# Performance work log

Hardware: AMD Instinct MI355X
Metric: run time of the kernel (lower is better)

## Reference

```python
import jax, jax.numpy as jnp
import numpy as np

B, P, D = 8, 1024, 1024
H, N = 16, 64  # num_heads, head_dim


def setup_inputs() -> dict:
    key = jax.random.key(0)
    k1, k2, k3 = jax.random.split(key, 3)
    inputs = jax.random.normal(k1, (B, P, D), dtype=jnp.float32)
    # Keras 'random_normal' initializer: stddev 0.05
    w_qkv = jax.random.normal(k2, (H, 3, D, N), dtype=jnp.float32) * 0.05
    w_o = jax.random.normal(k3, (N * H, D), dtype=jnp.float32) * 0.05
    return {"inputs": inputs, "w_qkv": w_qkv, "w_o": w_o}


def reference(inputs, w_qkv, w_o):
    # Per-head QKV projection: [b,p,d] x [h,3,d,n] -> [b,h,3,p,n]
    proj = jnp.einsum('bpv,havn->bhapn', inputs, w_qkv)
    q = proj[:, :, 0]  # [b,h,p,n]
    k = proj[:, :, 1]
    v = proj[:, :, 2]
    head_dim = q.shape[-1]
    scale = 1.0 / jnp.sqrt(jnp.asarray(head_dim, dtype=jnp.float32))
    scores = jnp.einsum('bhqn,bhkn->bhqk', q, k) * scale  # [b,h,p,p]
    attn = jax.nn.softmax(scores, axis=-1)
    out = jnp.einsum('bhqk,bhkn->bhqn', attn, v)  # [b,h,p,n]
    # concat heads along feature dim: [b,p,h*n]
    b, h, p, n = out.shape
    concat = out.transpose(0, 2, 1, 3).reshape(b, p, h * n)
    return jnp.einsum('bpi,ij->bpj', concat, w_o)  # [b,p,d_model]
```

## Files before the change

### kernel.cpp

```cpp
#include <hip/hip_runtime.h>
#include <stdint.h>

typedef _Float16 f16;
typedef __attribute__((ext_vector_type(2))) _Float16 f16x2;
typedef __attribute__((ext_vector_type(4))) _Float16 f16x4;
typedef __attribute__((ext_vector_type(8))) _Float16 f16x8;
typedef __attribute__((ext_vector_type(4))) float f32x4;
typedef __attribute__((ext_vector_type(4))) uint32_t u32x4;

__device__ __forceinline__ void gload_lds16(const void* g, void* l) {
  __builtin_amdgcn_global_load_lds(
      (__attribute__((address_space(1))) void*)const_cast<void*>(g),
      (__attribute__((address_space(3))) void*)l, 16, 0, 0);
}


__global__ void convert_x(const float* __restrict__ in, f16* __restrict__ out) {
  int i = blockIdx.x * 256 + threadIdx.x;
  float4 v = ((const float4*)in)[i];
  f16x4 hv;
  hv[0] = (f16)v.x; hv[1] = (f16)v.y; hv[2] = (f16)v.z; hv[3] = (f16)v.w;
  ((f16x4*)out)[i] = hv;
}

__global__ void transpose_wqkv(const float* __restrict__ in, f16* __restrict__ out) {
  __shared__ float tile[64][65];
  int s = blockIdx.x >> 4;
  int vt = blockIdx.x & 15;
  int hh = s / 3, a = s - hh * 3;
  int tx = threadIdx.x & 63, ty = threadIdx.x >> 6;
#pragma unroll
  for (int i = 0; i < 16; i++) {
    int r = i * 4 + ty;
    tile[r][tx] = in[((size_t)(s * 1024 + vt * 64 + r)) * 64 + tx];
  }
  __syncthreads();
#pragma unroll
  for (int i = 0; i < 16; i++) {
    int n = i * 4 + ty;
    out[((size_t)(a * 1024 + hh * 64 + n)) * 1024 + vt * 64 + tx] = (f16)tile[tx][n];
  }
}

__global__ void transpose_wo(const float* __restrict__ in, f16* __restrict__ out) {
  __shared__ float tile[64][65];
  int rt = blockIdx.x >> 4, ct = blockIdx.x & 15;
  int tx = threadIdx.x & 63, ty = threadIdx.x >> 6;
#pragma unroll
  for (int i = 0; i < 16; i++) {
    int r = i * 4 + ty;
    tile[r][tx] = in[((size_t)(rt * 64 + r)) * 1024 + ct * 64 + tx];
  }
  __syncthreads();
#pragma unroll
  for (int i = 0; i < 16; i++) {
    int j = i * 4 + ty;
    out[((size_t)(ct * 64 + j)) * 1024 + rt * 64 + tx] = (f16)tile[tx][j];
  }
}

__global__ __launch_bounds__(512, 2) void gemm_qkv_kernel(
    const f16* __restrict__ A, const f16* __restrict__ BT, f16* __restrict__ out,
    f16* __restrict__ VT) {
  constexpr int K = 1024;
  __shared__ __align__(16) f16 smem[73728];
  const int t = threadIdx.x;
  const int lane = t & 63, wave = t >> 6;
  const int lr = lane & 15, lg = lane >> 4;
  const int wm = wave >> 1, wn = wave & 1;
  const int bid = blockIdx.x;
  const int wg = (bid & 7) * 96 + (bid >> 3);
  const int bm = wg / 24, bn = wg % 24;
  const f16* Ab = A + (size_t)bm * 256 * K;
  const f16* Bb = BT + (size_t)bn * 128 * K;

  auto STAGE = [&](int kt, int buf) {
    const f16* srcA = Ab + kt * 64;
    char* dstA = (char*)(smem + buf * 16384);
#pragma unroll
    for (int i = 0; i < 4; i++) {
      int g = i * 512 + t;
      int r = g >> 3, p = g & 7;
      gload_lds16(srcA + (size_t)r * K + ((p ^ (r & 7)) << 3),
                  dstA + (i * 512 + wave * 64) * 16);
    }
    const f16* srcB = Bb + kt * 64;
    char* dstB = (char*)(smem + 49152 + buf * 8192);
#pragma unroll
    for (int i = 0; i < 2; i++) {
      int g = i * 512 + t;
      int r = g >> 3, p = g & 7;
      gload_lds16(srcB + (size_t)r * K + ((p ^ (r & 7)) << 3),
                  dstB + (i * 512 + wave * 64) * 16);
    }
  };

  const f32x4 zero4 = {0.f, 0.f, 0.f, 0.f};
  f32x4 acc[4][4];
#pragma unroll
  for (int m = 0; m < 4; m++)
#pragma unroll
    for (int n = 0; n < 4; n++) acc[m][n] = zero4;

  STAGE(0, 0);
  STAGE(1, 1);
  asm volatile("s_waitcnt vmcnt(6)" ::: "memory");
  __builtin_amdgcn_s_barrier();

  int cur = 0, nxt2 = 2;
#pragma unroll 1
  for (int kt = 0; kt < 16; kt++) {
    const f16* AL = smem + cur * 16384;
    const f16* BL = smem + 49152 + cur * 8192;

    if (kt + 2 < 16) STAGE(kt + 2, nxt2);

#pragma unroll
    for (int ks = 0; ks < 2; ks++) {
      f16x8 af[4], bf[4];
#pragma unroll
      for (int m = 0; m < 4; m++) {
        int r = wm * 64 + m * 16 + lr;
        af[m] = *(const f16x8*)&AL[r * 64 + (((ks * 4 + lg) ^ (r & 7)) << 3)];
      }
#pragma unroll
      for (int n = 0; n < 4; n++) {
        int rb = wn * 64 + n * 16 + lr;
        bf[n] = *(const f16x8*)&BL[rb * 64 + (((ks * 4 + lg) ^ (rb & 7)) << 3)];
      }
      __builtin_amdgcn_s_setprio(1);
#pragma unroll
      for (int m = 0; m < 4; m++)
#pragma unroll
        for (int n = 0; n < 4; n++)
          acc[m][n] = __builtin_amdgcn_mfma_f32_16x16x32_f16(af[m], bf[n], acc[m][n], 0, 0, 0);
      __builtin_amdgcn_s_setprio(0);
    }

    if (kt < 14) {
      asm volatile("s_waitcnt vmcnt(6)" ::: "memory");
    } else {
      asm volatile("s_waitcnt vmcnt(0)" ::: "memory");
    }
    __builtin_amdgcn_s_barrier();
    cur = (cur == 2) ? 0 : cur + 1;
    nxt2 = (nxt2 == 2) ? 0 : nxt2 + 1;
  }

  const int r0 = bm * 256 + wm * 64;
  const int c0 = bn * 128 + wn * 64;
  const int bb = bm >> 2;
#pragma unroll
  for (int m = 0; m < 4; m++) {
    int pl = (r0 + m * 16 + lg * 4) & 1023;
    int pl2 = (pl & 992) | ((pl & 12) << 1) | ((pl & 16) >> 2);
#pragma unroll
    for (int n = 0; n < 4; n++) {
      int gcb = c0 + n * 16;
      if (gcb >= 2048) {
        int vcol = gcb - 2048 + lr;
        f16x4 pv;
#pragma unroll
        for (int i = 0; i < 4; i++) pv[i] = (f16)acc[m][n][i];
        *(f16x4*)&VT[((size_t)(bb * 16 + (vcol >> 6)) * 64 + (vcol & 63)) * 1024 + pl2] = pv;
      } else {
#pragma unroll
        for (int i = 0; i < 4; i++) {
          int gr = r0 + m * 16 + lg * 4 + i;
          out[(size_t)gr * 3072 + gcb + lr] = (f16)acc[m][n][i];
        }
      }
    }
  }
}

__global__ __launch_bounds__(256, 2) void gemm_out_kernel(
    const f16* __restrict__ A, const f16* __restrict__ BT, float* __restrict__ out,
    int M, int N, int K) {
  __shared__ __align__(16) f16 As[128][64];
  __shared__ __align__(16) f16 Bs[128][64];
  const int t = threadIdx.x;
  const int lane = t & 63, wave = t >> 6;
  const int lr = lane & 15, lg = lane >> 4;
  const int wm = wave >> 1, wn = wave & 1;
  const int nTN = N >> 7;
  const int bm = blockIdx.x / nTN, bn = blockIdx.x % nTN;
  const f16* Ab = A + (size_t)bm * 128 * K;
  const f16* Bb = BT + (size_t)bn * 128 * K;

  const f32x4 zero4 = {0.f, 0.f, 0.f, 0.f};
  f32x4 acc[4][4];
#pragma unroll
  for (int m = 0; m < 4; m++)
#pragma unroll
    for (int n = 0; n < 4; n++) acc[m][n] = zero4;

  for (int k0 = 0; k0 < K; k0 += 64) {
    __syncthreads();
#pragma unroll
    for (int i = 0; i < 4; i++) {
      int q = wave * 4 + i;
      int u = q * 64 + lane;
      int r = u >> 3, j = u & 7;
      gload_lds16(Ab + (size_t)r * K + k0 + ((j ^ (r & 7)) << 3),
                  (char*)&As[0][0] + q * 1024);
      gload_lds16(Bb + (size_t)r * K + k0 + ((j ^ (r & 7)) << 3),
                  (char*)&Bs[0][0] + q * 1024);
    }
    __syncthreads();
#pragma unroll
    for (int half = 0; half < 2; half++) {
      f16x8 af[4], bf[4];
#pragma unroll
      for (int m = 0; m < 4; m++) {
        int r = wm * 64 + m * 16 + lr;
        af[m] = *(const f16x8*)&As[r][((half * 4 + lg) ^ (r & 7)) << 3];
      }
#pragma unroll
      for (int n = 0; n < 4; n++) {
        int r = wn * 64 + n * 16 + lr;
        bf[n] = *(const f16x8*)&Bs[r][((half * 4 + lg) ^ (r & 7)) << 3];
      }
#pragma unroll
      for (int m = 0; m < 4; m++)
#pragma unroll
        for (int n = 0; n < 4; n++)
          acc[m][n] = __builtin_amdgcn_mfma_f32_16x16x32_f16(af[m], bf[n], acc[m][n], 0, 0, 0);
    }
  }

  const int r0 = bm * 128 + wm * 64;
  const int c0 = bn * 128 + wn * 64;
#pragma unroll
  for (int m = 0; m < 4; m++)
#pragma unroll
    for (int n = 0; n < 4; n++)
#pragma unroll
      for (int i = 0; i < 4; i++) {
        int gr = r0 + m * 16 + lg * 4 + i;
        int gc = c0 + n * 16 + lr;
        out[(size_t)gr * N + gc] = acc[m][n][i];
      }
}

__global__ __launch_bounds__(256, 4) void attn_kernel(
    const f16* __restrict__ QKV, const f16* __restrict__ VT, f16* __restrict__ C) {
  __shared__ __align__(16) f16 smem[16384];

  const int t = threadIdx.x, lane = t & 63, wave = t >> 6;
  const int lr = lane & 15, lg = lane >> 4;
  const int bh = blockIdx.x, pt = blockIdx.y;
  const int b = bh >> 4, h = bh & 15;
  const int p0 = pt * 128;

  const f16* Qg = QKV + ((size_t)(b * 1024 + p0)) * 3072 + h * 64;
  const f16* Kg = QKV + ((size_t)(b * 1024)) * 3072 + 1024 + h * 64;
  const f16* Vg = VT + (size_t)bh * 64 * 1024;

#pragma unroll
  for (int i = 0; i < 4; i++) {
    int q = wave * 4 + i;
    int u = q * 64 + lane;
    int r = u >> 3, j = u & 7;
    gload_lds16(Qg + (size_t)r * 3072 + ((j ^ (r & 7)) << 3), (char*)smem + q * 1024);
  }
  __syncthreads();

  const f16 qscale = (f16)0.180336878f;
  f16x8 qa[2][2];
#pragma unroll
  for (int m = 0; m < 2; m++)
#pragma unroll
    for (int hh = 0; hh < 2; hh++) {
      int r = wave * 32 + m * 16 + lr;
      f16x8 v = *(const f16x8*)&smem[(size_t)r * 64 + (((hh * 4 + lg) ^ (lr & 7)) << 3)];
#pragma unroll
      for (int e = 0; e < 8; e++) v[e] *= qscale;
      qa[m][hh] = v;
    }
  __syncthreads();

  auto STAGE = [&](int kc, int cur) {
#pragma unroll
    for (int i = 0; i < 2; i++) {
      int q = wave * 2 + i;
      int u = q * 64 + lane;
      int r = u >> 3, j = u & 7;
      gload_lds16(Kg + (size_t)(kc * 64 + r) * 3072 + ((j ^ (r & 7)) << 3),
                  (char*)smem + cur * 16384 + q * 1024);
      gload_lds16(Vg + (size_t)r * 1024 + kc * 64 + ((j ^ (r & 7)) << 3),
                  (char*)smem + cur * 16384 + 8192 + q * 1024);
    }
  };

  STAGE(0, 0);
  STAGE(1, 1);
  __syncthreads();

  const f32x4 zero4 = {0.f, 0.f, 0.f, 0.f};
  f32x4 o[2][4], o_l[2];
#pragma unroll
  for (int m = 0; m < 2; m++) {
    o_l[m] = zero4;
#pragma unroll
    for (int n = 0; n < 4; n++) o[m][n] = zero4;
  }
  const f32x4 sInit = {-8.f, -8.f, -8.f, -8.f};
  const f16x8 ones8 = {(f16)1.f, (f16)1.f, (f16)1.f, (f16)1.f,
                       (f16)1.f, (f16)1.f, (f16)1.f, (f16)1.f};

#pragma unroll 1
  for (int kc = 0; kc < 16; kc++) {
    const int cur = kc & 1;
    const int kB = cur * 8192;
    const char* vB = (const char*)smem + cur * 16384 + 8192;

    f32x4 s[2][4];
#pragma unroll
    for (int m = 0; m < 2; m++)
#pragma unroll
      for (int kb = 0; kb < 4; kb++) s[m][kb] = sInit;
    __builtin_amdgcn_s_setprio(1);
#pragma unroll
    for (int kb = 0; kb < 4; kb++) {
      int r = kb * 16 + lr;
      f16x8 kf0 = *(const f16x8*)&smem[kB + (size_t)r * 64 + ((lg ^ (lr & 7)) << 3)];
      f16x8 kf1 = *(const f16x8*)&smem[kB + (size_t)r * 64 + (((4 + lg) ^ (lr & 7)) << 3)];
#pragma unroll
      for (int m = 0; m < 2; m++) {
        s[m][kb] = __builtin_amdgcn_mfma_f32_16x16x32_f16(kf0, qa[m][0], s[m][kb], 0, 0, 0);
        s[m][kb] = __builtin_amdgcn_mfma_f32_16x16x32_f16(kf1, qa[m][1], s[m][kb], 0, 0, 0);
      }
    }
    __builtin_amdgcn_s_setprio(0);

    f16x8 pa8[2][2];
#pragma unroll
    for (int m = 0; m < 2; m++)
#pragma unroll
      for (int j = 0; j < 2; j++) {
        uint32_t w0, w1, w2, w3;
        w0 = __builtin_bit_cast(uint32_t, __builtin_amdgcn_cvt_pkrtz(exp2f(s[m][2 * j][0]), exp2f(s[m][2 * j][1])));
        w1 = __builtin_bit_cast(uint32_t, __builtin_amdgcn_cvt_pkrtz(exp2f(s[m][2 * j][2]), exp2f(s[m][2 * j][3])));
        w2 = __builtin_bit_cast(uint32_t, __builtin_amdgcn_cvt_pkrtz(exp2f(s[m][2 * j + 1][0]), exp2f(s[m][2 * j + 1][1])));
        w3 = __builtin_bit_cast(uint32_t, __builtin_amdgcn_cvt_pkrtz(exp2f(s[m][2 * j + 1][2]), exp2f(s[m][2 * j + 1][3])));
        u32x4 ww = {w0, w1, w2, w3};
        pa8[m][j] = __builtin_bit_cast(f16x8, ww);
      }

    __builtin_amdgcn_s_setprio(1);
#pragma unroll
    for (int j = 0; j < 2; j++) {
      o_l[0] = __builtin_amdgcn_mfma_f32_16x16x32_f16(pa8[0][j], ones8, o_l[0], 0, 0, 0);
      o_l[1] = __builtin_amdgcn_mfma_f32_16x16x32_f16(pa8[1][j], ones8, o_l[1], 0, 0, 0);
#pragma unroll
      for (int n = 0; n < 4; n++) {
        int rv = n * 16 + lr;
        f16x8 vb = *(const f16x8*)(vB + (size_t)rv * 128 + (((4 * j + lg) ^ (lr & 7)) << 4));
        o[0][n] = __builtin_amdgcn_mfma_f32_16x16x32_f16(pa8[0][j], vb, o[0][n], 0, 0, 0);
        o[1][n] = __builtin_amdgcn_mfma_f32_16x16x32_f16(pa8[1][j], vb, o[1][n], 0, 0, 0);
      }
    }
    __builtin_amdgcn_s_setprio(0);

    __syncthreads();
    if (kc + 2 < 16) STAGE(kc + 2, cur);
  }

#pragma unroll
  for (int m = 0; m < 2; m++)
#pragma unroll
    for (int i = 0; i < 4; i++) {
      float li = 1.f / o_l[m][i];
      int prow = p0 + wave * 32 + m * 16 + lg * 4 + i;
#pragma unroll
      for (int n = 0; n < 4; n++) {
        int col = h * 64 + n * 16 + lr;
        C[((size_t)(b * 1024 + prow)) * 1024 + col] = (f16)(o[m][n][i] * li);
      }
    }
}

extern "C" void kernel_launch(void* const* d_in, const int* in_sizes, int n_in,
                              void* d_out, int out_size, void* d_ws, size_t ws_size,
                              hipStream_t stream) {
  const float* X = (const float*)d_in[0];
  const float* Wqkv = (const float*)d_in[1];
  const float* Wo = (const float*)d_in[2];
  float* Y = (float*)d_out;

  f16* ws = (f16*)d_ws;
  f16* X16 = ws;
  f16* WqkvT = ws + 8388608;
  f16* WoT = ws + 11534336;
  f16* QKV = ws + 12582912;
  f16* VT = (f16*)d_out;

  convert_x<<<8192, 256, 0, stream>>>(X, X16);
  transpose_wqkv<<<768, 256, 0, stream>>>(Wqkv, WqkvT);
  transpose_wo<<<256, 256, 0, stream>>>(Wo, WoT);
  gemm_qkv_kernel<<<768, 512, 0, stream>>>(X16, WqkvT, QKV, VT);
  attn_kernel<<<dim3(128, 8), 256, 0, stream>>>(QKV, VT, X16 );
  gemm_out_kernel<<<64 * 8, 256, 0, stream>>>(X16 , WoT, Y, 8192, 1024, 1024);
}
```

Before: 168.5 us.

## Fuse fp32-to-fp16 input conversion into QKV GEMM and simplify its tiling

Removes the standalone convert_x kernel and has the QKV projection GEMM load fp32 activations straight into LDS, converting to fp16 with packed round-toward-zero conversions at fragment load time. The GEMM is rewritten with 128x128 tiles, 256 threads, and a single-buffered syncthreads loop instead of the prior 3-stage async pipeline with 256-row tiles and block swizzling. This saves one full pass over the input activations but gives up load/compute overlap and doubles LDS bytes for the A tile.

```diff
diff --git a/kernel.cpp b/kernel.cpp
--- a/kernel.cpp
+++ b/kernel.cpp
@@ -15,14 +15,6 @@
 }
 
 
-__global__ void convert_x(const float* __restrict__ in, f16* __restrict__ out) {
-  int i = blockIdx.x * 256 + threadIdx.x;
-  float4 v = ((const float4*)in)[i];
-  f16x4 hv;
-  hv[0] = (f16)v.x; hv[1] = (f16)v.y; hv[2] = (f16)v.z; hv[3] = (f16)v.w;
-  ((f16x4*)out)[i] = hv;
-}
-
 __global__ void transpose_wqkv(const float* __restrict__ in, f16* __restrict__ out) {
   __shared__ float tile[64][65];
   int s = blockIdx.x >> 4;
@@ -59,41 +51,19 @@
   }
 }
 
-__global__ __launch_bounds__(512, 2) void gemm_qkv_kernel(
-    const f16* __restrict__ A, const f16* __restrict__ BT, f16* __restrict__ out,
+__global__ __launch_bounds__(256, 2) void gemm_qkv_kernel(
+    const float* __restrict__ A, const f16* __restrict__ BT, f16* __restrict__ out,
     f16* __restrict__ VT) {
   constexpr int K = 1024;
-  __shared__ __align__(16) f16 smem[73728];
+  __shared__ __align__(16) float Asf[128][64];
+  __shared__ __align__(16) f16 Bs[128][64];
   const int t = threadIdx.x;
   const int lane = t & 63, wave = t >> 6;
   const int lr = lane & 15, lg = lane >> 4;
   const int wm = wave >> 1, wn = wave & 1;
-  const int bid = blockIdx.x;
-  const int wg = (bid & 7) * 96 + (bid >> 3);
-  const int bm = wg / 24, bn = wg % 24;
-  const f16* Ab = A + (size_t)bm * 256 * K;
+  const int bm = blockIdx.x / 24, bn = blockIdx.x % 24;
+  const float* Ab = A + (size_t)bm * 128 * K;
   const f16* Bb = BT + (size_t)bn * 128 * K;
-
-  auto STAGE = [&](int kt, int buf) {
-    const f16* srcA = Ab + kt * 64;
-    char* dstA = (char*)(smem + buf * 16384);
-#pragma unroll
-    for (int i = 0; i < 4; i++) {
-      int g = i * 512 + t;
-      int r = g >> 3, p = g & 7;
-      gload_lds16(srcA + (size_t)r * K + ((p ^ (r & 7)) << 3),
-                  dstA + (i * 512 + wave * 64) * 16);
-    }
-    const f16* srcB = Bb + kt * 64;
-    char* dstB = (char*)(smem + 49152 + buf * 8192);
-#pragma unroll
-    for (int i = 0; i < 2; i++) {
-      int g = i * 512 + t;
-      int r = g >> 3, p = g & 7;
-      gload_lds16(srcB + (size_t)r * K + ((p ^ (r & 7)) << 3),
-                  dstB + (i * 512 + wave * 64) * 16);
-    }
-  };
 
   const f32x4 zero4 = {0.f, 0.f, 0.f, 0.f};
   f32x4 acc[4][4];
@@ -102,31 +72,43 @@
 #pragma unroll
     for (int n = 0; n < 4; n++) acc[m][n] = zero4;
 
-  STAGE(0, 0);
-  STAGE(1, 1);
-  asm volatile("s_waitcnt vmcnt(6)" ::: "memory");
-  __builtin_amdgcn_s_barrier();
-
-  int cur = 0, nxt2 = 2;
-#pragma unroll 1
-  for (int kt = 0; kt < 16; kt++) {
-    const f16* AL = smem + cur * 16384;
-    const f16* BL = smem + 49152 + cur * 8192;
-
-    if (kt + 2 < 16) STAGE(kt + 2, nxt2);
-
+  for (int k0 = 0; k0 < K; k0 += 64) {
+    __syncthreads();
+#pragma unroll
+    for (int i = 0; i < 8; i++) {
+      int g = i * 256 + t;
+      int r = g >> 4, j = g & 15;
+      gload_lds16(Ab + (size_t)r * K + k0 + ((j ^ (r & 15)) << 2),
+                  (char*)&Asf[0][0] + (i * 256 + wave * 64) * 16);
+    }
+#pragma unroll
+    for (int i = 0; i < 4; i++) {
+      int q = wave * 4 + i;
+      int u = q * 64 + lane;
+      int r = u >> 3, j = u & 7;
+      gload_lds16(Bb + (size_t)r * K + k0 + ((j ^ (r & 7)) << 3),
+                  (char*)&Bs[0][0] + q * 1024);
+    }
+    __syncthreads();
 #pragma unroll
     for (int ks = 0; ks < 2; ks++) {
       f16x8 af[4], bf[4];
 #pragma unroll
       for (int m = 0; m < 4; m++) {
         int r = wm * 64 + m * 16 + lr;
-        af[m] = *(const f16x8*)&AL[r * 64 + (((ks * 4 + lg) ^ (r & 7)) << 3)];
-      }
-#pragma unroll
-      for (int n = 0; n < 4; n++) {
-        int rb = wn * 64 + n * 16 + lr;
-        bf[n] = *(const f16x8*)&BL[rb * 64 + (((ks * 4 + lg) ^ (rb & 7)) << 3)];
+        f32x4 a0 = *(const f32x4*)&Asf[r][((2 * (ks * 4 + lg) + 0) ^ (r & 15)) << 2];
+        f32x4 a1 = *(const f32x4*)&Asf[r][((2 * (ks * 4 + lg) + 1) ^ (r & 15)) << 2];
+        uint32_t w0 = __builtin_bit_cast(uint32_t, __builtin_amdgcn_cvt_pkrtz(a0[0], a0[1]));
+        uint32_t w1 = __builtin_bit_cast(uint32_t, __builtin_amdgcn_cvt_pkrtz(a0[2], a0[3]));
+        uint32_t w2 = __builtin_bit_cast(uint32_t, __builtin_amdgcn_cvt_pkrtz(a1[0], a1[1]));
+        uint32_t w3 = __builtin_bit_cast(uint32_t, __builtin_amdgcn_cvt_pkrtz(a1[2], a1[3]));
+        u32x4 ww = {w0, w1, w2, w3};
+        af[m] = __builtin_bit_cast(f16x8, ww);
+      }
+#pragma unroll
+      for (int n = 0; n < 4; n++) {
+        int r = wn * 64 + n * 16 + lr;
+        bf[n] = *(const f16x8*)&Bs[r][((ks * 4 + lg) ^ (r & 7)) << 3];
       }
       __builtin_amdgcn_s_setprio(1);
 #pragma unroll
@@ -136,41 +118,36 @@
           acc[m][n] = __builtin_amdgcn_mfma_f32_16x16x32_f16(af[m], bf[n], acc[m][n], 0, 0, 0);
       __builtin_amdgcn_s_setprio(0);
     }
-
-    if (kt < 14) {
-      asm volatile("s_waitcnt vmcnt(6)" ::: "memory");
-    } else {
-      asm volatile("s_waitcnt vmcnt(0)" ::: "memory");
-    }
-    __builtin_amdgcn_s_barrier();
-    cur = (cur == 2) ? 0 : cur + 1;
-    nxt2 = (nxt2 == 2) ? 0 : nxt2 + 1;
-  }
-
-  const int r0 = bm * 256 + wm * 64;
+  }
+
+  const int r0 = bm * 128 + wm * 64;
   const int c0 = bn * 128 + wn * 64;
-  const int bb = bm >> 2;
-#pragma unroll
-  for (int m = 0; m < 4; m++) {
-    int pl = (r0 + m * 16 + lg * 4) & 1023;
-    int pl2 = (pl & 992) | ((pl & 12) << 1) | ((pl & 16) >> 2);
-#pragma unroll
-    for (int n = 0; n < 4; n++) {
-      int gcb = c0 + n * 16;
-      if (gcb >= 2048) {
-        int vcol = gcb - 2048 + lr;
+  if (bn >= 16) {
+    const int bb = bm >> 3;
+#pragma unroll
+    for (int m = 0; m < 4; m++) {
+      int pl = (r0 + m * 16 + lg * 4) & 1023;
+      int pl2 = (pl & 992) | ((pl & 12) << 1) | ((pl & 16) >> 2);
+#pragma unroll
+      for (int n = 0; n < 4; n++) {
+        int vcol = c0 - 2048 + n * 16 + lr;
         f16x4 pv;
 #pragma unroll
         for (int i = 0; i < 4; i++) pv[i] = (f16)acc[m][n][i];
         *(f16x4*)&VT[((size_t)(bb * 16 + (vcol >> 6)) * 64 + (vcol & 63)) * 1024 + pl2] = pv;
-      } else {
+      }
+    }
+  } else {
+#pragma unroll
+    for (int m = 0; m < 4; m++)
+#pragma unroll
+      for (int n = 0; n < 4; n++)
 #pragma unroll
         for (int i = 0; i < 4; i++) {
           int gr = r0 + m * 16 + lg * 4 + i;
-          out[(size_t)gr * 3072 + gcb + lr] = (f16)acc[m][n][i];
+          int gc = c0 + n * 16 + lr;
+          out[(size_t)gr * 3072 + gc] = (f16)acc[m][n][i];
         }
-      }
-    }
   }
 }
 
@@ -390,16 +367,15 @@
   float* Y = (float*)d_out;
 
   f16* ws = (f16*)d_ws;
-  f16* X16 = ws;
+  f16* C16 = ws;
   f16* WqkvT = ws + 8388608;
   f16* WoT = ws + 11534336;
   f16* QKV = ws + 12582912;
   f16* VT = (f16*)d_out;
 
-  convert_x<<<8192, 256, 0, stream>>>(X, X16);
   transpose_wqkv<<<768, 256, 0, stream>>>(Wqkv, WqkvT);
   transpose_wo<<<256, 256, 0, stream>>>(Wo, WoT);
-  gemm_qkv_kernel<<<768, 512, 0, stream>>>(X16, WqkvT, QKV, VT);
-  attn_kernel<<<dim3(128, 8), 256, 0, stream>>>(QKV, VT, X16 );
-  gemm_out_kernel<<<64 * 8, 256, 0, stream>>>(X16 , WoT, Y, 8192, 1024, 1024);
-}
+  gemm_qkv_kernel<<<64 * 24, 256, 0, stream>>>(X, WqkvT, QKV, VT);
+  attn_kernel<<<dim3(128, 8), 256, 0, stream>>>(QKV, VT, C16);
+  gemm_out_kernel<<<64 * 8, 256, 0, stream>>>(C16, WoT, Y, 8192, 1024, 1024);
+}
```

After: 166.9 us. Within noise of the previous version (-0.9%).
